# Performance work log

Hardware: AMD Instinct MI355X
Metric: run time of the kernel (lower is better)

## Reference

```python
import jax, jax.numpy as jnp
import numpy as np

D_MODEL = 2048
N_HEADS = 16
HEAD_DIM = D_MODEL // N_HEADS  # 128
SCALE_BASE = 512


def rotate_half(x):
    x1, x2 = jnp.split(x, 2, axis=-1)
    return jnp.concatenate((-x2, x1), axis=-1)


def rotary_xpos(seq_len, dim, dtype=jnp.float32):
    inv_freq = 1.0 / (10000.0 ** (jnp.arange(0, dim, 2, dtype=jnp.float32) / dim))
    t = jnp.arange(seq_len, dtype=jnp.float32)
    freqs = jnp.einsum('i,j->ij', t, inv_freq)
    freqs = jnp.concatenate((freqs, freqs), axis=-1)  # [S, dim]
    scale_base = (jnp.arange(0, dim, 2, dtype=jnp.float32) + 0.4 * dim) / (1.4 * dim)
    power = (t - seq_len // 2) / SCALE_BASE
    scale = scale_base[None, :] ** power[:, None]  # [S, dim/2]
    scale = jnp.concatenate((scale, scale), axis=-1)  # [S, dim]
    return freqs.astype(dtype), scale.astype(dtype)


def apply_rotary(t, pos, scale):
    return t * jnp.cos(pos) * scale + rotate_half(t) * jnp.sin(pos) * scale


def setup_inputs() -> dict:
    key = jax.random.key(0)
    ks = jax.random.split(key, 5)
    B, S = 2, 2048
    hidden_states = jax.random.normal(ks[0], (B, S, D_MODEL), dtype=jnp.float32)
    # Linear weights stored as [out, in] like torch; we use x @ W.T
    w_q = jax.random.normal(ks[1], (N_HEADS * HEAD_DIM, D_MODEL), dtype=jnp.float32) * 0.02
    w_kv = jax.random.normal(ks[2], (2 * HEAD_DIM, D_MODEL), dtype=jnp.float32) * 0.02
    w_proj = jax.random.normal(ks[3], (D_MODEL, N_HEADS * HEAD_DIM), dtype=jnp.float32) * 0.02
    b_proj = jax.random.normal(ks[4], (D_MODEL,), dtype=jnp.float32) * 0.02
    return {"hidden_states": hidden_states, "w_q": w_q, "w_kv": w_kv,
            "w_proj": w_proj, "b_proj": b_proj}


def reference(hidden_states, w_q, w_kv, w_proj, b_proj):
    B, S, _ = hidden_states.shape
    q = hidden_states @ w_q.T                      # [B,S,H*D]
    kv = hidden_states @ w_kv.T                    # [B,S,2*D]
    k, v = jnp.split(kv, 2, axis=-1)               # [B,S,D] each
    q = q.reshape(B, S, N_HEADS, HEAD_DIM).transpose(0, 2, 1, 3)  # [B,H,S,D]

    scale_w = HEAD_DIM ** (-0.5)
    q = q * scale_w
    k = k * scale_w

    pos, xscale = rotary_xpos(S, HEAD_DIM, q.dtype)
    q = apply_rotary(q, pos, xscale)               # broadcast [S,D] over [B,H,S,D]
    k = apply_rotary(k, pos, 1.0 / xscale)         # [B,S,D]

    attn = jnp.einsum('bnih,bjh->bnij', q, k)      # [B,H,S,S]
    causal = jnp.triu(jnp.ones((S, S), dtype=bool), 1)
    attn = jnp.where(causal, -jnp.finfo(attn.dtype).max, attn)
    attn = jax.nn.softmax(attn, axis=-1)

    out = jnp.einsum('bnij,bjd->bind', attn, v)    # [B,S,H,D]
    out = out.reshape(B, S, N_HEADS * HEAD_DIM)
    out = out @ w_proj.T + b_proj
    return out
```

## Files before the change

kernel.cpp:

```cpp
#include <hip/hip_runtime.h>
#include <math.h>

typedef __bf16 bf16;
typedef __bf16 bf16x8 __attribute__((ext_vector_type(8)));
typedef float f32x4 __attribute__((ext_vector_type(4)));

#define MFMA16(a, b, c) __builtin_amdgcn_mfma_f32_16x16x32_bf16((a), (b), (c), 0, 0, 0)

__device__ __forceinline__ float clampf(float v, float lo, float hi) {
  return fminf(fmaxf(v, lo), hi);
}

__device__ __forceinline__ void async_copy16(const void* g, void* l) {
  __builtin_amdgcn_global_load_lds(
      (__attribute__((address_space(1))) void*)g,
      (__attribute__((address_space(3))) void*)l,
      16, 0, 0);
}


__global__ void convert_bf16(const float* __restrict__ hs,
                             const float* __restrict__ wq,
                             const float* __restrict__ wkv,
                             const float* __restrict__ wproj,
                             bf16* __restrict__ hs_bf,
                             bf16* __restrict__ wqkv_bf,
                             bf16* __restrict__ wproj_bf) {
  const long long v = (long long)blockIdx.x * blockDim.x + threadIdx.x;
  const float* src;
  bf16* dst;
  long long off;
  if (v < 1048576) { src = hs; dst = hs_bf; off = v; }
  else if (v < 1572864) { src = wq; dst = wqkv_bf; off = v - 1048576; }
  else if (v < 1638400) { src = wkv; dst = wqkv_bf + 4194304; off = v - 1572864; }
  else { src = wproj; dst = wproj_bf; off = v - 1638400; }
  const f32x4* p = (const f32x4*)(src + off * 8);
  f32x4 f0 = p[0], f1 = p[1];
  bf16x8 r;
#pragma unroll
  for (int i = 0; i < 4; ++i) { r[i] = (bf16)f0[i]; r[i + 4] = (bf16)f1[i]; }
  *(bf16x8*)(dst + off * 8) = r;
}

__global__ __launch_bounds__(256, 2)
void gemm_qkv(const bf16* __restrict__ A, const bf16* __restrict__ Bw,
              bf16* __restrict__ Cq, bf16* __restrict__ Ckv) {
  const int K = 2048;
  __shared__ bf16 As[128 * 32];
  __shared__ bf16 Bs[128 * 32];
  const int tid = threadIdx.x;
  const int wave = tid >> 6, lane = tid & 63;
  const int quad = lane >> 4, l15 = lane & 15;
  const int r4 = lane >> 2, c4 = lane & 3;
  const int wm = wave >> 1, wn = wave & 1;
  const int orig = blockIdx.x + 18 * blockIdx.y;
  const int wgid = (orig & 7) * 72 + (orig >> 3);
  const int bx = wgid % 18;
  const int bm = (wgid / 18) * 128;
  const bf16* Bp = Bw + (size_t)bx * 128 * K;

  const f32x4 vzero = {0.f, 0.f, 0.f, 0.f};
  f32x4 acc[4][4];
#pragma unroll
  for (int i = 0; i < 4; ++i)
#pragma unroll
    for (int j = 0; j < 4; ++j) acc[i][j] = vzero;

  for (int kt = 0; kt < K; kt += 32) {
    __syncthreads();
#pragma unroll
    for (int q = 0; q < 2; ++q) {
      const int chunk = wave * 2 + q;
      const int row = chunk * 16 + r4;
      async_copy16(A + (size_t)(bm + row) * K + kt + c4 * 8, (char*)As + chunk * 1024);
      async_copy16(Bp + (size_t)row * K + kt + c4 * 8, (char*)Bs + chunk * 1024);
    }
    __syncthreads();
    bf16x8 af[4], bfr[4];
#pragma unroll
    for (int i = 0; i < 4; ++i)
      af[i] = *(const bf16x8*)((const char*)As + (wm * 64 + i * 16 + l15) * 64 + quad * 16);
#pragma unroll
    for (int i = 0; i < 4; ++i)
      bfr[i] = *(const bf16x8*)((const char*)Bs + (wn * 64 + i * 16 + l15) * 64 + quad * 16);
#pragma unroll
    for (int mi = 0; mi < 4; ++mi)
#pragma unroll
      for (int ni = 0; ni < 4; ++ni)
        acc[mi][ni] = MFMA16(af[mi], bfr[ni], acc[mi][ni]);
  }

  bf16* Cp;
  int ldc, cn;
  if (bx < 16) { Cp = Cq; ldc = 2048; cn = bx * 128; }
  else { Cp = Ckv; ldc = 256; cn = (bx - 16) * 128; }
#pragma unroll
  for (int mi = 0; mi < 4; ++mi)
#pragma unroll
    for (int ni = 0; ni < 4; ++ni) {
      const int col = cn + wn * 64 + ni * 16 + l15;
#pragma unroll
      for (int r = 0; r < 4; ++r) {
        const int row = bm + wm * 64 + mi * 16 + quad * 4 + r;
        Cp[(size_t)row * ldc + col] = (bf16)clampf(acc[mi][ni][r], -1000.f, 1000.f);
      }
    }
}

__global__ __launch_bounds__(256, 2)
void gemm_proj(const bf16* __restrict__ A, const bf16* __restrict__ Bw,
               const float* __restrict__ bias, float* __restrict__ C) {
  const int K = 2048;
  __shared__ bf16 As[128 * 32];
  __shared__ bf16 Bs[128 * 32];
  const int tid = threadIdx.x;
  const int wave = tid >> 6, lane = tid & 63;
  const int quad = lane >> 4, l15 = lane & 15;
  const int r4 = lane >> 2, c4 = lane & 3;
  const int wm = wave >> 1, wn = wave & 1;
  const int orig = blockIdx.x + 16 * blockIdx.y;
  const int wgid = (orig & 7) * 64 + (orig >> 3);
  const int bn = (wgid % 16) * 128;
  const int bm = (wgid / 16) * 128;
  const bf16* Bp = Bw + (size_t)bn * K;

  const f32x4 vzero = {0.f, 0.f, 0.f, 0.f};
  f32x4 acc[4][4];
#pragma unroll
  for (int i = 0; i < 4; ++i)
#pragma unroll
    for (int j = 0; j < 4; ++j) acc[i][j] = vzero;

  for (int kt = 0; kt < K; kt += 32) {
    __syncthreads();
#pragma unroll
    for (int q = 0; q < 2; ++q) {
      const int chunk = wave * 2 + q;
      const int row = chunk * 16 + r4;
      async_copy16(A + (size_t)(bm + row) * K + kt + c4 * 8, (char*)As + chunk * 1024);
      async_copy16(Bp + (size_t)row * K + kt + c4 * 8, (char*)Bs + chunk * 1024);
    }
    __syncthreads();
    bf16x8 af[4], bfr[4];
#pragma unroll
    for (int i = 0; i < 4; ++i)
      af[i] = *(const bf16x8*)((const char*)As + (wm * 64 + i * 16 + l15) * 64 + quad * 16);
#pragma unroll
    for (int i = 0; i < 4; ++i)
      bfr[i] = *(const bf16x8*)((const char*)Bs + (wn * 64 + i * 16 + l15) * 64 + quad * 16);
#pragma unroll
    for (int mi = 0; mi < 4; ++mi)
#pragma unroll
      for (int ni = 0; ni < 4; ++ni)
        acc[mi][ni] = MFMA16(af[mi], bfr[ni], acc[mi][ni]);
  }

#pragma unroll
  for (int mi = 0; mi < 4; ++mi)
#pragma unroll
    for (int ni = 0; ni < 4; ++ni) {
      const int col = bn + wn * 64 + ni * 16 + l15;
      const float bv = bias[col];
#pragma unroll
      for (int r = 0; r < 4; ++r) {
        const int row = bm + wm * 64 + mi * 16 + quad * 4 + r;
        C[(size_t)row * 2048 + col] = clampf(acc[mi][ni][r] + bv, -1000.f, 1000.f);
      }
    }
}

__global__ void rotary_kernel(bf16* __restrict__ Cq, bf16* __restrict__ Ckv,
                              bf16* __restrict__ VT) {
  const int row = blockIdx.x;
  const int b = row >> 11, s = row & 2047;
  const int t = threadIdx.x;
  const float power = (float)(s - 1024) * (1.0f / 512.0f);
  const float scale_w = 0.08838834764831845f;
  const float k_if = 0.2076205059304679f;

  const int h = t >> 4;
  const int j0 = (t & 15) * 4;
  const size_t qbase = (size_t)row * 2048 + (size_t)h * 128;
#pragma unroll
  for (int u = 0; u < 4; ++u) {
    const int j = j0 + u;
    const float pos = (float)s * exp2f(-k_if * (float)j);
    const float c = cosf(pos), sn = sinf(pos);
    const float sb = ((float)(2 * j) + 51.2f) * (1.0f / 179.2f);
    const float xs = exp2f(power * log2f(sb));
    const float f = xs * scale_w;
    const float q1 = (float)Cq[qbase + j];
    const float q2 = (float)Cq[qbase + j + 64];
    Cq[qbase + j]      = (bf16)((q1 * c - q2 * sn) * f);
    Cq[qbase + j + 64] = (bf16)((q2 * c + q1 * sn) * f);
  }

  if (t < 64) {
    const int j = t;
    const float pos = (float)s * exp2f(-k_if * (float)j);
    const float c = cosf(pos), sn = sinf(pos);
    const float sb = ((float)(2 * j) + 51.2f) * (1.0f / 179.2f);
    const float xs = exp2f(power * log2f(sb));
    const float f = scale_w / xs;
    const size_t kvb = (size_t)row * 256;
    const float k1 = (float)Ckv[kvb + j];
    const float k2 = (float)Ckv[kvb + j + 64];
    Ckv[kvb + j]      = (bf16)((k1 * c - k2 * sn) * f);
    Ckv[kvb + j + 64] = (bf16)((k2 * c + k1 * sn) * f);
  } else if (t < 128) {
    const int d = (t - 64) * 2;
    const size_t kvb = (size_t)row * 256 + 128;
    VT[((size_t)b * 128 + d) * 2048 + s]     = Ckv[kvb + d];
    VT[((size_t)b * 128 + d + 1) * 2048 + s] = Ckv[kvb + d + 1];
  }
}

__global__ __launch_bounds__(256, 2)
void flash_attn(const bf16* __restrict__ Qp, const bf16* __restrict__ Kkv,
                const bf16* __restrict__ VT, bf16* __restrict__ O) {
  __shared__ bf16 Ks[2][4 * 64 * 32];
  __shared__ bf16 Vs[2][2 * 128 * 32];
  __shared__ bf16 Ps[4][1024];

  const int tid = threadIdx.x;
  const int wave = tid >> 6, lane = tid & 63;
  const int quad = lane >> 4, l15 = lane & 15;
  const int r4 = lane >> 2, c4 = lane & 3;
  const int bh = blockIdx.x, b = bh >> 4, h = bh & 15;
  const int y = blockIdx.y;
  const int nkvA = y + 1;
  const int wrow = wave * 16;

  const int ssw = (r4 >> 1) & 3;
  const int rsw = ((l15 >> 1) & 3) * 16;

  const bf16* Kb = Kkv + (size_t)b * 2048 * 256;
  const bf16* Vb = VT + (size_t)b * 128 * 2048;

  bf16x8 vones;
  {
    const bf16 ov = (bf16)((l15 == 0) ? 1.0f : 0.0f);
#pragma unroll
    for (int i = 0; i < 8; ++i) vones[i] = ov;
  }

  const f32x4 vzero = {0.f, 0.f, 0.f, 0.f};
  bf16x8 qa[4];
  f32x4 oacc[8];
  f32x4 lacc;

  auto load_q = [&](int q0) {
#pragma unroll
    for (int ks = 0; ks < 4; ++ks)
      qa[ks] = *(const bf16x8*)(Qp + ((size_t)(b * 2048 + q0 + wrow + l15)) * 2048 +
                                h * 128 + ks * 32 + quad * 8);
  };
  auto reset_acc = [&]() {
    lacc = vzero;
#pragma unroll
    for (int n8 = 0; n8 < 8; ++n8) oacc[n8] = vzero;
  };

  auto stage = [&](int kv0, int buf) {
#pragma unroll
    for (int t = 0; t < 4; ++t) {
      const int ii = wave * 4 + t;
      const int p = ii >> 2, ch = ii & 3;
      async_copy16(Kb + (size_t)(kv0 + ch * 16 + r4) * 256 + p * 32 + (c4 ^ ssw) * 8,
                   (char*)Ks[buf] + ii * 1024);
    }
#pragma unroll
    for (int t = 0; t < 4; ++t) {
      const int ii = wave * 4 + t;
      const int pc = ii >> 3, ch = ii & 7;
      async_copy16(Vb + (size_t)(ch * 16 + r4) * 2048 + kv0 + pc * 32 + (c4 ^ ssw) * 8,
                   (char*)Vs[buf] + ii * 1024);
    }
  };

  auto epilogue = [&](int q0) {
#pragma unroll
    for (int r = 0; r < 4; ++r) {
      const float l = __shfl(lacc[r], lane & 48);
      const float inv = 1.0f / l;
      const int s = q0 + wrow + quad * 4 + r;
#pragma unroll
      for (int n8 = 0; n8 < 8; ++n8) {
        const int d = n8 * 16 + l15;
        O[((size_t)(b * 2048 + s)) * 2048 + h * 128 + d] = (bf16)(oacc[n8][r] * inv);
      }
    }
  };

  int q0 = y * 64;
  load_q(q0);
  reset_acc();
  stage(0, 0);

  for (int jt = 0; jt < 33; ++jt) {
    const int kv0 = (jt < nkvA ? jt : jt - nkvA) * 64;
    const int buf = jt & 1;
    __syncthreads();
    if (jt + 1 < 33) {
      const int njt = jt + 1;
      stage((njt < nkvA ? njt : njt - nkvA) * 64, buf ^ 1);
    }

    if (kv0 <= q0 + wrow + 15) {
      f32x4 sacc[4];
#pragma unroll
      for (int ns = 0; ns < 4; ++ns) sacc[ns] = vzero;
      __builtin_amdgcn_s_setprio(1);
#pragma unroll
      for (int ks = 0; ks < 4; ++ks) {
        bf16x8 kb[4];
#pragma unroll
        for (int ns = 0; ns < 4; ++ns)
          kb[ns] = *(const bf16x8*)((const char*)Ks[buf] + ks * 4096 +
                                    (ns * 16 + l15) * 64 + (quad * 16 ^ rsw));
#pragma unroll
        for (int ns = 0; ns < 4; ++ns)
          sacc[ns] = MFMA16(qa[ks], kb[ns], sacc[ns]);
      }
      __builtin_amdgcn_s_setprio(0);
      if (kv0 + 63 > q0 + wrow) {
#pragma unroll
        for (int ns = 0; ns < 4; ++ns)
#pragma unroll
          for (int r = 0; r < 4; ++r) {
            const int qg = q0 + wrow + quad * 4 + r;
            const int kg = kv0 + ns * 16 + l15;
            sacc[ns][r] = (kg > qg) ? 0.0f : __expf(sacc[ns][r]);
          }
      } else {
#pragma unroll
        for (int ns = 0; ns < 4; ++ns)
#pragma unroll
          for (int r = 0; r < 4; ++r)
            sacc[ns][r] = __expf(sacc[ns][r]);
      }
#pragma unroll
      for (int ns = 0; ns < 4; ++ns)
#pragma unroll
        for (int r = 0; r < 4; ++r) {
          const int row = quad * 4 + r;
          const int slot = (ns & 1) * 2 + (l15 >> 3);
          *(bf16*)((char*)Ps[wave] + (ns >> 1) * 1024 + row * 64 +
                   ((slot ^ ((row >> 1) & 3)) * 16) + (l15 & 7) * 2) = (bf16)sacc[ns][r];
        }
#pragma unroll
      for (int ks2 = 0; ks2 < 2; ++ks2) {
        bf16x8 pa, vb[8];
        pa = *(const bf16x8*)((const char*)Ps[wave] + ks2 * 1024 + l15 * 64 +
                              (quad * 16 ^ rsw));
#pragma unroll
        for (int n8 = 0; n8 < 8; ++n8)
          vb[n8] = *(const bf16x8*)((const char*)Vs[buf] + ks2 * 8192 +
                                    (n8 * 16 + l15) * 64 + (quad * 16 ^ rsw));
        __builtin_amdgcn_s_setprio(1);
#pragma unroll
        for (int n8 = 0; n8 < 8; ++n8)
          oacc[n8] = MFMA16(pa, vb[n8], oacc[n8]);
        lacc = MFMA16(pa, vones, lacc);
        __builtin_amdgcn_s_setprio(0);
      }
    }

    if (jt == nkvA - 1) {
      epilogue(q0);
      reset_acc();
      q0 = (31 - y) * 64;
      load_q(q0);
    }
  }
  epilogue(q0);
}

extern "C" void kernel_launch(void* const* d_in, const int* in_sizes, int n_in,
                              void* d_out, int out_size, void* d_ws, size_t ws_size,
                              hipStream_t stream) {
  const float* hs     = (const float*)d_in[0];
  const float* w_q    = (const float*)d_in[1];
  const float* w_kv   = (const float*)d_in[2];
  const float* w_proj = (const float*)d_in[3];
  const float* b_proj = (const float*)d_in[4];
  float* out = (float*)d_out;
  bf16* Qbuf  = (bf16*)d_out;
  bf16* hs_bf = (bf16*)((char*)d_out + 16777216);

  char* ws = (char*)d_ws;
  bf16* Ckv      = (bf16*)(ws);
  bf16* VT       = (bf16*)(ws + 2097152);
  bf16* AO       = (bf16*)(ws + 3145728);
  bf16* wqkv_bf  = (bf16*)(ws + 19922944);
  bf16* wproj_bf = (bf16*)(ws + 29360128);

  convert_bf16<<<dim3(8448), dim3(256), 0, stream>>>(hs, w_q, w_kv, w_proj,
                                                     hs_bf, wqkv_bf, wproj_bf);
  gemm_qkv<<<dim3(18, 32), dim3(256), 0, stream>>>(hs_bf, wqkv_bf, Qbuf, Ckv);
  rotary_kernel<<<dim3(4096), dim3(256), 0, stream>>>(Qbuf, Ckv, VT);
  flash_attn<<<dim3(32, 16), dim3(256), 0, stream>>>(Qbuf, Ckv, VT, AO);
  gemm_proj<<<dim3(16, 32), dim3(256), 0, stream>>>(AO, wproj_bf, b_proj, out);
}
```

Baseline: 272.8 us.

## Rewrite flash attention with 32x32 MFMA, register-resident P, and two-wave blocks

Switches the attention kernel from 16x16x32 to 32x32x16 bf16 MFMA tiles and computes S transposed (K as the A operand). This keeps the exp'd probabilities in registers, converting them with cvt_pk and permlane32 swaps instead of writing them through LDS. The row-sum now accumulates in scalar registers instead of an extra ones-MFMA. Blocks shrink to 128 threads (2 waves of 32 query rows each) with new XOR-swizzled K/V staging. This cuts LDS traffic and MFMA issue count, at the cost of higher register pressure, lower wave count per block, and launch bounds of 1.

```diff
diff --git a/kernel.cpp b/kernel.cpp
--- a/kernel.cpp
+++ b/kernel.cpp
@@ -4,8 +4,10 @@
 typedef __bf16 bf16;
 typedef __bf16 bf16x8 __attribute__((ext_vector_type(8)));
 typedef float f32x4 __attribute__((ext_vector_type(4)));
+typedef float f32x16 __attribute__((ext_vector_type(16)));
 
 #define MFMA16(a, b, c) __builtin_amdgcn_mfma_f32_16x16x32_bf16((a), (b), (c), 0, 0, 0)
+#define MFMA32(a, b, c) __builtin_amdgcn_mfma_f32_32x32x16_bf16((a), (b), (c), 0, 0, 0)
 
 __device__ __forceinline__ float clampf(float v, float lo, float hi) {
   return fminf(fmaxf(v, lo), hi);
@@ -16,6 +18,32 @@
       (__attribute__((address_space(1))) void*)g,
       (__attribute__((address_space(3))) void*)l,
       16, 0, 0);
+}
+
+__device__ __forceinline__ unsigned cvtpk(float a, float b) {
+  unsigned r;
+  asm("v_cvt_pk_bf16_f32 %0, %1, %2" : "=v"(r) : "v"(a), "v"(b));
+  return r;
+}
+
+__device__ __forceinline__ void pl32swap(unsigned& a, unsigned& b, int hi) {
+#if __has_builtin(__builtin_amdgcn_permlane32_swap)
+  auto r = __builtin_amdgcn_permlane32_swap(a, b, false, false);
+  a = r[0];
+  b = r[1];
+#else
+  unsigned ax = (unsigned)__shfl_xor((int)a, 32, 64);
+  unsigned bx = (unsigned)__shfl_xor((int)b, 32, 64);
+  unsigned o0 = hi ? bx : a;
+  unsigned o1 = hi ? b : ax;
+  a = o0; b = o1;
+#endif
+}
+
+__device__ __forceinline__ bf16x8 frag4(unsigned d0, unsigned d1, unsigned d2, unsigned d3) {
+  union { unsigned u[4]; bf16x8 v; } t;
+  t.u[0] = d0; t.u[1] = d1; t.u[2] = d2; t.u[3] = d3;
+  return t.v;
 }
 
 
@@ -215,81 +243,75 @@
   }
 }
 
-__global__ __launch_bounds__(256, 2)
+__global__ __launch_bounds__(128, 1)
 void flash_attn(const bf16* __restrict__ Qp, const bf16* __restrict__ Kkv,
                 const bf16* __restrict__ VT, bf16* __restrict__ O) {
-  __shared__ bf16 Ks[2][4 * 64 * 32];
-  __shared__ bf16 Vs[2][2 * 128 * 32];
-  __shared__ bf16 Ps[4][1024];
+  __shared__ bf16 Ks[2][64 * 128];
+  __shared__ bf16 Vs[2][128 * 64];
 
   const int tid = threadIdx.x;
   const int wave = tid >> 6, lane = tid & 63;
-  const int quad = lane >> 4, l15 = lane & 15;
-  const int r4 = lane >> 2, c4 = lane & 3;
+  const int hi = lane >> 5, l31 = lane & 31, l15 = lane & 15, l7 = lane & 7;
   const int bh = blockIdx.x, b = bh >> 4, h = bh & 15;
   const int y = blockIdx.y;
   const int nkvA = y + 1;
-  const int wrow = wave * 16;
-
-  const int ssw = (r4 >> 1) & 3;
-  const int rsw = ((l15 >> 1) & 3) * 16;
+  const int wrow = wave * 32;
 
   const bf16* Kb = Kkv + (size_t)b * 2048 * 256;
   const bf16* Vb = VT + (size_t)b * 128 * 2048;
 
-  bf16x8 vones;
-  {
-    const bf16 ov = (bf16)((l15 == 0) ? 1.0f : 0.0f);
-#pragma unroll
-    for (int i = 0; i < 8; ++i) vones[i] = ov;
-  }
-
-  const f32x4 vzero = {0.f, 0.f, 0.f, 0.f};
-  bf16x8 qa[4];
-  f32x4 oacc[8];
-  f32x4 lacc;
+  f32x16 sacc[2];
+  f32x16 oacc[4];
+  bf16x8 qb[8];
+  float lacc;
+  const f32x16 vz16 = {0.f, 0.f, 0.f, 0.f, 0.f, 0.f, 0.f, 0.f,
+                       0.f, 0.f, 0.f, 0.f, 0.f, 0.f, 0.f, 0.f};
 
   auto load_q = [&](int q0) {
 #pragma unroll
-    for (int ks = 0; ks < 4; ++ks)
-      qa[ks] = *(const bf16x8*)(Qp + ((size_t)(b * 2048 + q0 + wrow + l15)) * 2048 +
-                                h * 128 + ks * 32 + quad * 8);
+    for (int ks = 0; ks < 8; ++ks)
+      qb[ks] = *(const bf16x8*)(Qp + ((size_t)(b * 2048 + q0 + wrow + l31)) * 2048 +
+                                h * 128 + ks * 16 + hi * 8);
   };
   auto reset_acc = [&]() {
-    lacc = vzero;
-#pragma unroll
-    for (int n8 = 0; n8 < 8; ++n8) oacc[n8] = vzero;
+    lacc = 0.f;
+#pragma unroll
+    for (int nt = 0; nt < 4; ++nt) oacc[nt] = vz16;
   };
 
   auto stage = [&](int kv0, int buf) {
 #pragma unroll
-    for (int t = 0; t < 4; ++t) {
-      const int ii = wave * 4 + t;
-      const int p = ii >> 2, ch = ii & 3;
-      async_copy16(Kb + (size_t)(kv0 + ch * 16 + r4) * 256 + p * 32 + (c4 ^ ssw) * 8,
+    for (int t = 0; t < 8; ++t) {
+      const int ii = wave * 8 + t;
+      const int kvr = ii * 4 + (lane >> 4);
+      async_copy16(Kb + (size_t)(kv0 + kvr) * 256 + 8 * ((lane & 15) ^ (kvr & 15)),
                    (char*)Ks[buf] + ii * 1024);
     }
 #pragma unroll
-    for (int t = 0; t < 4; ++t) {
-      const int ii = wave * 4 + t;
-      const int pc = ii >> 3, ch = ii & 7;
-      async_copy16(Vb + (size_t)(ch * 16 + r4) * 2048 + kv0 + pc * 32 + (c4 ^ ssw) * 8,
-                   (char*)Vs[buf] + ii * 1024);
+    for (int t = 0; t < 8; ++t) {
+      const int jj = wave * 8 + t;
+      const int dr = jj * 8 + (lane >> 3);
+      async_copy16(Vb + (size_t)dr * 2048 + kv0 + 8 * ((lane & 7) ^ (dr & 7)),
+                   (char*)Vs[buf] + jj * 1024);
     }
   };
 
   auto epilogue = [&](int q0) {
-#pragma unroll
-    for (int r = 0; r < 4; ++r) {
-      const float l = __shfl(lacc[r], lane & 48);
-      const float inv = 1.0f / l;
-      const int s = q0 + wrow + quad * 4 + r;
-#pragma unroll
-      for (int n8 = 0; n8 < 8; ++n8) {
-        const int d = n8 * 16 + l15;
-        O[((size_t)(b * 2048 + s)) * 2048 + h * 128 + d] = (bf16)(oacc[n8][r] * inv);
-      }
-    }
+    const float lt = lacc + __shfl_xor(lacc, 32, 64);
+    const float linv = 1.0f / lt;
+    float li[16];
+#pragma unroll
+    for (int r = 0; r < 16; ++r)
+      li[r] = __shfl(linv, (r & 3) + 8 * (r >> 2) + 4 * hi, 64);
+#pragma unroll
+    for (int nt = 0; nt < 4; ++nt)
+#pragma unroll
+      for (int r = 0; r < 16; ++r) {
+        const int qr = (r & 3) + 8 * (r >> 2) + 4 * hi;
+        const int s = q0 + wrow + qr;
+        O[((size_t)(b * 2048 + s)) * 2048 + h * 128 + nt * 32 + l31] =
+            (bf16)(oacc[nt][r] * li[r]);
+      }
   };
 
   int q0 = y * 64;
@@ -306,64 +328,71 @@
       stage((njt < nkvA ? njt : njt - nkvA) * 64, buf ^ 1);
     }
 
-    if (kv0 <= q0 + wrow + 15) {
-      f32x4 sacc[4];
-#pragma unroll
-      for (int ns = 0; ns < 4; ++ns) sacc[ns] = vzero;
+    if (kv0 <= q0 + wrow + 31) {
+      sacc[0] = vz16;
+      sacc[1] = vz16;
       __builtin_amdgcn_s_setprio(1);
 #pragma unroll
-      for (int ks = 0; ks < 4; ++ks) {
-        bf16x8 kb[4];
-#pragma unroll
-        for (int ns = 0; ns < 4; ++ns)
-          kb[ns] = *(const bf16x8*)((const char*)Ks[buf] + ks * 4096 +
-                                    (ns * 16 + l15) * 64 + (quad * 16 ^ rsw));
-#pragma unroll
-        for (int ns = 0; ns < 4; ++ns)
-          sacc[ns] = MFMA16(qa[ks], kb[ns], sacc[ns]);
+      for (int ks = 0; ks < 8; ++ks) {
+        const int sl = ((2 * ks + hi) ^ l15) << 4;
+        bf16x8 ka0 = *(const bf16x8*)((const char*)Ks[buf] + l31 * 256 + sl);
+        bf16x8 ka1 = *(const bf16x8*)((const char*)Ks[buf] + (32 + l31) * 256 + sl);
+        sacc[0] = MFMA32(ka0, qb[ks], sacc[0]);
+        sacc[1] = MFMA32(ka1, qb[ks], sacc[1]);
       }
       __builtin_amdgcn_s_setprio(0);
+
+      const int qg = q0 + wrow + l31;
+      float p[32];
       if (kv0 + 63 > q0 + wrow) {
 #pragma unroll
-        for (int ns = 0; ns < 4; ++ns)
-#pragma unroll
-          for (int r = 0; r < 4; ++r) {
-            const int qg = q0 + wrow + quad * 4 + r;
-            const int kg = kv0 + ns * 16 + l15;
-            sacc[ns][r] = (kg > qg) ? 0.0f : __expf(sacc[ns][r]);
+        for (int mt = 0; mt < 2; ++mt)
+#pragma unroll
+          for (int r = 0; r < 16; ++r) {
+            const int kg = kv0 + mt * 32 + (r & 3) + 8 * (r >> 2) + 4 * hi;
+            p[mt * 16 + r] = (kg > qg) ? 0.0f : __expf(sacc[mt][r]);
           }
       } else {
 #pragma unroll
-        for (int ns = 0; ns < 4; ++ns)
-#pragma unroll
-          for (int r = 0; r < 4; ++r)
-            sacc[ns][r] = __expf(sacc[ns][r]);
-      }
-#pragma unroll
-      for (int ns = 0; ns < 4; ++ns)
-#pragma unroll
-        for (int r = 0; r < 4; ++r) {
-          const int row = quad * 4 + r;
-          const int slot = (ns & 1) * 2 + (l15 >> 3);
-          *(bf16*)((char*)Ps[wave] + (ns >> 1) * 1024 + row * 64 +
-                   ((slot ^ ((row >> 1) & 3)) * 16) + (l15 & 7) * 2) = (bf16)sacc[ns][r];
+        for (int mt = 0; mt < 2; ++mt)
+#pragma unroll
+          for (int r = 0; r < 16; ++r)
+            p[mt * 16 + r] = __expf(sacc[mt][r]);
+      }
+#pragma unroll
+      for (int i = 0; i < 32; ++i) lacc += p[i];
+
+      bf16x8 pa[4];
+#pragma unroll
+      for (int mt = 0; mt < 2; ++mt) {
+        const int o = mt * 16;
+        unsigned a0 = cvtpk(p[o + 0], p[o + 1]);
+        unsigned b0 = cvtpk(p[o + 4], p[o + 5]);
+        pl32swap(a0, b0, hi);
+        unsigned a1 = cvtpk(p[o + 2], p[o + 3]);
+        unsigned b1 = cvtpk(p[o + 6], p[o + 7]);
+        pl32swap(a1, b1, hi);
+        pa[mt * 2 + 0] = frag4(a0, a1, b0, b1);
+        unsigned a2 = cvtpk(p[o + 8], p[o + 9]);
+        unsigned b2 = cvtpk(p[o + 12], p[o + 13]);
+        pl32swap(a2, b2, hi);
+        unsigned a3 = cvtpk(p[o + 10], p[o + 11]);
+        unsigned b3 = cvtpk(p[o + 14], p[o + 15]);
+        pl32swap(a3, b3, hi);
+        pa[mt * 2 + 1] = frag4(a2, a3, b2, b3);
+      }
+
+      __builtin_amdgcn_s_setprio(1);
+#pragma unroll
+      for (int ks = 0; ks < 4; ++ks) {
+        const int sl = ((2 * ks + hi) ^ l7) << 4;
+#pragma unroll
+        for (int nt = 0; nt < 4; ++nt) {
+          bf16x8 vb = *(const bf16x8*)((const char*)Vs[buf] + (nt * 32 + l31) * 128 + sl);
+          oacc[nt] = MFMA32(pa[ks], vb, oacc[nt]);
         }
-#pragma unroll
-      for (int ks2 = 0; ks2 < 2; ++ks2) {
-        bf16x8 pa, vb[8];
-        pa = *(const bf16x8*)((const char*)Ps[wave] + ks2 * 1024 + l15 * 64 +
-                              (quad * 16 ^ rsw));
-#pragma unroll
-        for (int n8 = 0; n8 < 8; ++n8)
-          vb[n8] = *(const bf16x8*)((const char*)Vs[buf] + ks2 * 8192 +
-                                    (n8 * 16 + l15) * 64 + (quad * 16 ^ rsw));
-        __builtin_amdgcn_s_setprio(1);
-#pragma unroll
-        for (int n8 = 0; n8 < 8; ++n8)
-          oacc[n8] = MFMA16(pa, vb[n8], oacc[n8]);
-        lacc = MFMA16(pa, vones, lacc);
-        __builtin_amdgcn_s_setprio(0);
-      }
+      }
+      __builtin_amdgcn_s_setprio(0);
     }
 
     if (jt == nkvA - 1) {
@@ -399,6 +428,6 @@
                                                      hs_bf, wqkv_bf, wproj_bf);
   gemm_qkv<<<dim3(18, 32), dim3(256), 0, stream>>>(hs_bf, wqkv_bf, Qbuf, Ckv);
   rotary_kernel<<<dim3(4096), dim3(256), 0, stream>>>(Qbuf, Ckv, VT);
-  flash_attn<<<dim3(32, 16), dim3(256), 0, stream>>>(Qbuf, Ckv, VT, AO);
+  flash_attn<<<dim3(32, 16), dim3(128), 0, stream>>>(Qbuf, Ckv, VT, AO);
   gemm_proj<<<dim3(16, 32), dim3(256), 0, stream>>>(AO, wproj_bf, b_proj, out);
 }
```

After: 288.0 us. +5.6%, slower.
